# Kernel tuning notes

Measured on AMD Instinct MI355X. Metric: run time of the kernel, lower is better.

Reference implementation:

```python
import jax, jax.numpy as jnp
import numpy as np

N = 100000
E = 1600000
D_IN = 50
D_H = 128
D_OUT = 128
EPS = 1e-5


def setup_inputs() -> dict:
    key = jax.random.key(0)
    ks = jax.random.split(key, 24)
    def w(k, shape, fan_in):
        return jax.random.normal(k, shape, jnp.float32) / np.sqrt(fan_in)
    inp = {
        'x': jax.random.normal(ks[0], (N, D_IN), jnp.float32),
        'edge_src': jax.random.randint(ks[1], (E,), 0, N, jnp.int32),
        'edge_dst': jax.random.randint(ks[2], (E,), 0, N, jnp.int32),
        # SAGEConv 1: D_IN -> D_H
        'Wl1': w(ks[3], (D_IN, D_H), D_IN), 'Wr1': w(ks[4], (D_IN, D_H), D_IN), 'b1': jnp.zeros((D_H,), jnp.float32),
        # SAGEConv 2: D_H -> D_H
        'Wl2': w(ks[5], (D_H, D_H), D_H), 'Wr2': w(ks[6], (D_H, D_H), D_H), 'b2': jnp.zeros((D_H,), jnp.float32),
        # SAGEConv 3: D_H -> D_OUT
        'Wl3': w(ks[7], (D_H, D_OUT), D_H), 'Wr3': w(ks[8], (D_H, D_OUT), D_H), 'b3': jnp.zeros((D_OUT,), jnp.float32),
        # skip linears (no bias)
        'Ws1': w(ks[9], (D_IN, D_H), D_IN), 'Ws2': w(ks[10], (D_IN, D_H), D_IN),
        # LayerNorm affine
        'lnw1': jnp.ones((D_H,), jnp.float32), 'lnb1': jnp.zeros((D_H,), jnp.float32),
        'lnw2': jnp.ones((D_H,), jnp.float32), 'lnb2': jnp.zeros((D_H,), jnp.float32),
        'lnw3': jnp.ones((D_OUT,), jnp.float32), 'lnb3': jnp.zeros((D_OUT,), jnp.float32),
        # PReLU scalar slopes (PyG init 0.25)
        'a1': jnp.float32(0.25), 'a2': jnp.float32(0.25), 'a3': jnp.float32(0.25),
    }
    return inp


def _sage(x, src, dst, Wl, Wr, b):
    # mean aggregation of source features at destinations, then linear + root
    msg = x[src]                                              # [E, d]
    agg = jax.ops.segment_sum(msg, dst, num_segments=N)       # [N, d]
    cnt = jax.ops.segment_sum(jnp.ones((src.shape[0],), x.dtype), dst, num_segments=N)
    mean = agg / jnp.maximum(cnt, 1.0)[:, None]
    return mean @ Wl + x @ Wr + b


def _graph_ln(x, w, b):
    # PyG LayerNorm mode='graph', batch=None: normalize over all nodes+channels
    xc = x - jnp.mean(x)
    std = jnp.sqrt(jnp.mean(xc * xc))
    return (xc / (std + EPS)) * w + b


def _prelu(x, a):
    return jnp.where(x >= 0, x, a * x)


def reference(x, edge_src, edge_dst, Wl1, Wr1, b1, Wl2, Wr2, b2, Wl3, Wr3, b3,
              Ws1, Ws2, lnw1, lnb1, lnw2, lnb2, lnw3, lnb3, a1, a2, a3):
    h1 = _sage(x, edge_src, edge_dst, Wl1, Wr1, b1)
    h1 = _prelu(_graph_ln(h1, lnw1, lnb1), a1)
    h2 = _sage(h1 + x @ Ws1, edge_src, edge_dst, Wl2, Wr2, b2)
    h2 = _prelu(_graph_ln(h2, lnw2, lnb2), a2)
    ret = _sage(h1 + h2 + x @ Ws2, edge_src, edge_dst, Wl3, Wr3, b3)
    ret = _prelu(_graph_ln(ret, lnw3, lnb3), a3)
    return ret
```

## Files before the change

kernel.cpp:

```cpp
#include <hip/hip_runtime.h>

#define D_IN 50
#define LN_EPS 1e-5f
#define BSH 8
#define MAXB 512

typedef __bf16 bf16_t;
typedef bf16_t bf16x8 __attribute__((ext_vector_type(8)));
typedef bf16_t bf16x4 __attribute__((ext_vector_type(4)));
typedef bf16_t bf16x2 __attribute__((ext_vector_type(2)));
typedef float f32x4_t __attribute__((ext_vector_type(4)));

__global__ void bucket_hist_k(const int* __restrict__ dst, int* __restrict__ bcnt,
                              int e, int nb) {
    __shared__ int lh[MAXB];
    int t = threadIdx.x;
    for (int i = t; i < nb; i += 256) lh[i] = 0;
    __syncthreads();
    for (int i = blockIdx.x * 256 + t; i < e; i += gridDim.x * 256)
        atomicAdd(&lh[dst[i] >> BSH], 1);
    __syncthreads();
    for (int i = t; i < nb; i += 256) {
        int c = lh[i];
        if (c) atomicAdd(&bcnt[i * 16], c);
    }
}

__global__ void bscan_k(const int* __restrict__ bcnt, int* __restrict__ boff,
                        int* __restrict__ bpos, int nb, int e) {
    __shared__ int l[MAXB];
    int t = threadIdx.x;
    l[t] = (t < nb) ? bcnt[t * 16] : 0;
    __syncthreads();
    for (int off = 1; off < MAXB; off <<= 1) {
        int v = (t >= off) ? l[t - off] : 0;
        __syncthreads();
        l[t] += v;
        __syncthreads();
    }
    int excl = (t > 0) ? l[t - 1] : 0;
    if (t < nb) { boff[t] = excl; bpos[t * 16] = excl; }
    if (t == 0) boff[nb] = e;
}

__global__ void scatter_k(const int* __restrict__ src, const int* __restrict__ dst,
                          int* __restrict__ bpos, unsigned* __restrict__ pool,
                          int e, int nb) {
    __shared__ int lh[MAXB];
    __shared__ int lcur[MAXB];
    int t = threadIdx.x;
    for (int i = t; i < nb; i += 256) lh[i] = 0;
    __syncthreads();
    int chunk = (e + gridDim.x - 1) / gridDim.x;
    int s = blockIdx.x * chunk;
    int en = min(e, s + chunk);
    for (int i = s + t; i < en; i += 256)
        atomicAdd(&lh[dst[i] >> BSH], 1);
    __syncthreads();
    for (int i = t; i < nb; i += 256) {
        int c = lh[i];
        lcur[i] = c ? atomicAdd(&bpos[i * 16], c) : 0;
    }
    __syncthreads();
    for (int i = s + t; i < en; i += 256) {
        int d = dst[i];
        int p = atomicAdd(&lcur[d >> BSH], 1);
        pool[p] = (unsigned)src[i] | ((unsigned)(d & 255) << 17);
    }
}

__global__ void nhist_k(const unsigned* __restrict__ pool, const int* __restrict__ boff,
                        int* __restrict__ cnt, int n) {
    __shared__ int lc[256];
    int b = blockIdx.x, t = threadIdx.x;
    lc[t] = 0;
    __syncthreads();
    int s = boff[b], e = boff[b + 1];
    for (int i = s + t; i < e; i += 256) atomicAdd(&lc[pool[i] >> 17], 1);
    __syncthreads();
    int nd = (b << BSH) + t;
    if (nd < n) cnt[nd] = lc[t];
}

__global__ void scan_partial_k(const int* __restrict__ cnt, int* __restrict__ part, int n) {
    __shared__ int lds[256];
    int base = blockIdx.x * 1024;
    int t = threadIdx.x;
    int s = 0;
    for (int j = 0; j < 4; j++) {
        int idx = base + t * 4 + j;
        if (idx < n) s += cnt[idx];
    }
    lds[t] = s;
    __syncthreads();
    for (int off = 128; off > 0; off >>= 1) {
        if (t < off) lds[t] += lds[t + off];
        __syncthreads();
    }
    if (t == 0) part[blockIdx.x] = lds[0];
}

__global__ void scan_root_k(int* part, int nb) {
    if (threadIdx.x == 0 && blockIdx.x == 0) {
        int run = 0;
        for (int i = 0; i < nb; i++) { int v = part[i]; part[i] = run; run += v; }
    }
}

__global__ void scan_final_k(const int* __restrict__ cnt, const int* __restrict__ part,
                             int* __restrict__ row_ptr, int n) {
    __shared__ int lds[256];
    int base = blockIdx.x * 1024;
    int t = threadIdx.x;
    int v[4];
    int s = 0;
    for (int j = 0; j < 4; j++) {
        int idx = base + t * 4 + j;
        v[j] = (idx < n) ? cnt[idx] : 0;
        s += v[j];
    }
    lds[t] = s;
    __syncthreads();
    for (int off = 1; off < 256; off <<= 1) {
        int xv = (t >= off) ? lds[t - off] : 0;
        __syncthreads();
        lds[t] += xv;
        __syncthreads();
    }
    int ex = (t > 0 ? lds[t - 1] : 0) + part[blockIdx.x];
    for (int j = 0; j < 4; j++) {
        int idx = base + t * 4 + j;
        if (idx < n) {
            row_ptr[idx] = ex;
            if (idx == n - 1) row_ptr[n] = ex + v[j];
            ex += v[j];
        }
    }
}

__global__ void cfill_k(const unsigned* __restrict__ pool, const int* __restrict__ boff,
                        const int* __restrict__ rp, int* __restrict__ col, int n) {
    __shared__ int lpos[256];
    int b = blockIdx.x, t = threadIdx.x;
    int nd = (b << BSH) + t;
    lpos[t] = (nd < n) ? rp[nd] : 0;
    __syncthreads();
    int s = boff[b], e = boff[b + 1];
    for (int i = s + t; i < e; i += 256) {
        unsigned pk = pool[i];
        int slot = atomicAdd(&lpos[pk >> 17], 1);
        col[slot] = (int)(pk & 0x1FFFFu);
    }
}

struct ConvDesc { const float* w; bf16_t* o; int kin; int kpad; };
struct ConvArgs { ConvDesc d[8]; };

__global__ void conv_w_k(ConvArgs args) {
    ConvDesc d = args.d[blockIdx.y];
    int i = blockIdx.x * 256 + threadIdx.x;
    int tot = 128 * d.kpad;
    if (i >= tot) return;
    int n = i / d.kpad, k = i - n * d.kpad;
    float v = (k < d.kin) ? d.w[(size_t)k * 128 + n] : 0.f;
    d.o[i] = (bf16_t)v;
}

__global__ void conv_x_k(const float* __restrict__ x, bf16_t* __restrict__ xb, int n) {
    int i = blockIdx.x * 256 + threadIdx.x;
    if (i >= n * 64) return;
    int node = i >> 6, k = i & 63;
    xb[i] = (k < D_IN) ? (bf16_t)x[node * D_IN + k] : (bf16_t)0.f;
}

__global__ void agg_bf64_k(const bf16_t* __restrict__ feat, const int* __restrict__ rp,
                           const int* __restrict__ col, bf16_t* __restrict__ mean, int n) {
    int wid = (blockIdx.x * blockDim.x + threadIdx.x) >> 6;
    int lane = threadIdx.x & 63;
    if (wid >= n) return;
    int start = rp[wid], end = rp[wid + 1];
    float a0 = 0.f, a1 = 0.f;
    int e = start;
    for (; e + 3 < end; e += 4) {
        int s0 = col[e], s1 = col[e + 1], s2 = col[e + 2], s3 = col[e + 3];
        float v0 = (float)feat[(size_t)s0 * 64 + lane];
        float v1 = (float)feat[(size_t)s1 * 64 + lane];
        float v2 = (float)feat[(size_t)s2 * 64 + lane];
        float v3 = (float)feat[(size_t)s3 * 64 + lane];
        a0 += v0 + v1;
        a1 += v2 + v3;
    }
    for (; e < end; e++) a0 += (float)feat[(size_t)col[e] * 64 + lane];
    int c = end - start;
    float invc = 1.f / (float)(c > 0 ? c : 1);
    mean[(size_t)wid * 64 + lane] = (bf16_t)((a0 + a1) * invc);
}

__global__ void agg_bf128_k(const bf16_t* __restrict__ feat, const int* __restrict__ rp,
                            const int* __restrict__ col, bf16_t* __restrict__ mean, int n) {
    int wid = (blockIdx.x * blockDim.x + threadIdx.x) >> 6;
    int lane = threadIdx.x & 63;
    if (wid >= n) return;
    int start = rp[wid], end = rp[wid + 1];
    float ax0 = 0.f, ay0 = 0.f, ax1 = 0.f, ay1 = 0.f;
    int e = start;
    for (; e + 3 < end; e += 4) {
        int s0 = col[e], s1 = col[e + 1], s2 = col[e + 2], s3 = col[e + 3];
        bf16x2 v0 = *(const bf16x2*)(feat + (size_t)s0 * 128 + lane * 2);
        bf16x2 v1 = *(const bf16x2*)(feat + (size_t)s1 * 128 + lane * 2);
        bf16x2 v2 = *(const bf16x2*)(feat + (size_t)s2 * 128 + lane * 2);
        bf16x2 v3 = *(const bf16x2*)(feat + (size_t)s3 * 128 + lane * 2);
        ax0 += (float)v0.x + (float)v1.x;
        ay0 += (float)v0.y + (float)v1.y;
        ax1 += (float)v2.x + (float)v3.x;
        ay1 += (float)v2.y + (float)v3.y;
    }
    for (; e < end; e++) {
        bf16x2 v0 = *(const bf16x2*)(feat + (size_t)col[e] * 128 + lane * 2);
        ax0 += (float)v0.x;
        ay0 += (float)v0.y;
    }
    int c = end - start;
    float invc = 1.f / (float)(c > 0 ? c : 1);
    bf16x2 o;
    o.x = (bf16_t)((ax0 + ax1) * invc);
    o.y = (bf16_t)((ay0 + ay1) * invc);
    *(bf16x2*)(mean + (size_t)wid * 128 + lane * 2) = o;
}

template <int KPAD, bool DUAL, bool ACC>
__global__ __launch_bounds__(256) void mfma_gemm_k(
    const bf16_t* __restrict__ A, const bf16_t* __restrict__ B,
    const bf16_t* __restrict__ WlT, const bf16_t* __restrict__ WrT,
    const float* __restrict__ bias,
    bf16_t* __restrict__ out, float2* __restrict__ partials, int M) {
    constexpr int KC = KPAD / 32;
    constexpr int WELE = 8 * KC * 64 * 8;
    __shared__ bf16_t lwl[WELE];
    __shared__ bf16_t lwr[DUAL ? WELE : 8];

    const int tid = threadIdx.x;
    for (int ch = tid; ch < 8 * KC * 64; ch += 256) {
        int nt = ch / (KC * 64);
        int rem = ch - nt * (KC * 64);
        int c = rem >> 6;
        int ln = rem & 63;
        int m = ln & 15, q = ln >> 4;
        size_t srcoff = (size_t)(nt * 16 + m) * KPAD + c * 32 + q * 8;
        *(bf16x8*)&lwl[ch * 8] = *(const bf16x8*)(WlT + srcoff);
        if (DUAL) *(bf16x8*)&lwr[ch * 8] = *(const bf16x8*)(WrT + srcoff);
    }
    __syncthreads();

    const int wid = blockIdx.x * 4 + (tid >> 6);
    const int lane = tid & 63;
    const int row0 = wid * 32;
    if (row0 >= M) return;
    const int m = lane & 15;
    const int q = lane >> 4;

    bf16x8 af[2][KC], bfr[DUAL ? 2 : 1][DUAL ? KC : 1];
#pragma unroll
    for (int s = 0; s < 2; s++) {
        const bf16_t* ar = A + (size_t)(row0 + s * 16 + m) * KPAD + q * 8;
#pragma unroll
        for (int c = 0; c < KC; c++) af[s][c] = *(const bf16x8*)(ar + c * 32);
        if (DUAL) {
            const bf16_t* br = B + (size_t)(row0 + s * 16 + m) * KPAD + q * 8;
#pragma unroll
            for (int c = 0; c < KC; c++) bfr[s][c] = *(const bf16x8*)(br + c * 32);
        }
    }

    float lsum = 0.f, lsum2 = 0.f;
#pragma unroll
    for (int nt = 0; nt < 8; nt++) {
        f32x4_t acc0 = {0.f, 0.f, 0.f, 0.f};
        f32x4_t acc1 = {0.f, 0.f, 0.f, 0.f};
#pragma unroll
        for (int c = 0; c < KC; c++) {
            bf16x8 w = *(const bf16x8*)&lwl[((nt * KC + c) * 64 + lane) * 8];
            acc0 = __builtin_amdgcn_mfma_f32_16x16x32_bf16(af[0][c], w, acc0, 0, 0, 0);
            acc1 = __builtin_amdgcn_mfma_f32_16x16x32_bf16(af[1][c], w, acc1, 0, 0, 0);
        }
        if (DUAL) {
#pragma unroll
            for (int c = 0; c < KC; c++) {
                bf16x8 w = *(const bf16x8*)&lwr[((nt * KC + c) * 64 + lane) * 8];
                acc0 = __builtin_amdgcn_mfma_f32_16x16x32_bf16(bfr[0][c], w, acc0, 0, 0, 0);
                acc1 = __builtin_amdgcn_mfma_f32_16x16x32_bf16(bfr[1][c], w, acc1, 0, 0, 0);
            }
        }
        float bv = bias ? bias[nt * 16 + m] : 0.f;
#pragma unroll
        for (int s = 0; s < 2; s++) {
            f32x4_t* ap = (s == 0) ? &acc0 : &acc1;
#pragma unroll
            for (int r = 0; r < 4; r++) {
                int row = row0 + s * 16 + q * 4 + r;
                if (row < M) {
                    float o = (*ap)[r] + bv;
                    out[(size_t)row * 128 + nt * 16 + m] = (bf16_t)o;
                    if (ACC) { lsum += o; lsum2 += o * o; }
                }
            }
        }
    }
    if (ACC) {
        for (int off = 32; off > 0; off >>= 1) {
            lsum += __shfl_down(lsum, off);
            lsum2 += __shfl_down(lsum2, off);
        }
        if (lane == 0) partials[wid] = make_float2(lsum, lsum2);
    }
}

__global__ void reduce_partials_k(const float2* __restrict__ p, int n,
                                  double* __restrict__ outp) {
    __shared__ double s1[256], s2[256];
    int t = threadIdx.x;
    double a = 0.0, b = 0.0;
    for (int i = t; i < n; i += 256) { a += (double)p[i].x; b += (double)p[i].y; }
    s1[t] = a; s2[t] = b;
    __syncthreads();
    for (int off = 128; off > 0; off >>= 1) {
        if (t < off) { s1[t] += s1[t + off]; s2[t] += s2[t + off]; }
        __syncthreads();
    }
    if (t == 0) { outp[0] = s1[0]; outp[1] = s2[0]; }
}

template <int MODE>
__global__ void ln_prelu_k(const bf16_t* __restrict__ pre, const bf16_t* __restrict__ h1in,
                           const bf16_t* __restrict__ s,
                           const float* __restrict__ lnw, const float* __restrict__ lnb,
                           const float* __restrict__ a_ptr, const double* __restrict__ acc,
                           void* __restrict__ out0v, void* __restrict__ out1v, int total) {
    int i = blockIdx.x * blockDim.x + threadIdx.x;
    if (i * 4 >= total) return;
    double cinv = 1.0 / (double)total;
    double mm = acc[0] * cinv;
    double var = acc[1] * cinv - mm * mm;
    float stdv = (float)sqrt(var > 0.0 ? var : 0.0);
    float scale = 1.0f / (stdv + LN_EPS);
    float mf = (float)mm;
    float a = a_ptr[0];
    int c4 = i & 31;
    float4 w = ((const float4*)lnw)[c4];
    float4 b = ((const float4*)lnb)[c4];
    bf16x4 p4 = ((const bf16x4*)pre)[i];
    float4 h;
    h.x = ((float)p4.x - mf) * scale * w.x + b.x;
    h.y = ((float)p4.y - mf) * scale * w.y + b.y;
    h.z = ((float)p4.z - mf) * scale * w.z + b.z;
    h.w = ((float)p4.w - mf) * scale * w.w + b.w;
    h.x = h.x >= 0.f ? h.x : a * h.x;
    h.y = h.y >= 0.f ? h.y : a * h.y;
    h.z = h.z >= 0.f ? h.z : a * h.z;
    h.w = h.w >= 0.f ? h.w : a * h.w;
    if (MODE == 1) {
        bf16x4 hb;
        hb.x = (bf16_t)h.x; hb.y = (bf16_t)h.y; hb.z = (bf16_t)h.z; hb.w = (bf16_t)h.w;
        ((bf16x4*)out0v)[i] = hb;
        bf16x4 sv = ((const bf16x4*)s)[i];
        bf16x4 tb;
        tb.x = (bf16_t)(h.x + (float)sv.x); tb.y = (bf16_t)(h.y + (float)sv.y);
        tb.z = (bf16_t)(h.z + (float)sv.z); tb.w = (bf16_t)(h.w + (float)sv.w);
        ((bf16x4*)out1v)[i] = tb;
    } else if (MODE == 2) {
        bf16x4 hv = ((const bf16x4*)h1in)[i];
        bf16x4 sv = ((const bf16x4*)s)[i];
        bf16x4 tb;
        tb.x = (bf16_t)((float)hv.x + h.x + (float)sv.x);
        tb.y = (bf16_t)((float)hv.y + h.y + (float)sv.y);
        tb.z = (bf16_t)((float)hv.z + h.z + (float)sv.z);
        tb.w = (bf16_t)((float)hv.w + h.w + (float)sv.w);
        ((bf16x4*)out0v)[i] = tb;
    } else {
        ((float4*)out0v)[i] = h;
    }
}

extern "C" void kernel_launch(void* const* d_in, const int* in_sizes, int n_in,
                              void* d_out, int out_size, void* d_ws, size_t ws_size,
                              hipStream_t stream) {
    const float* x    = (const float*)d_in[0];
    const int*   esrc = (const int*)d_in[1];
    const int*   edst = (const int*)d_in[2];
    const float* Wl1  = (const float*)d_in[3];
    const float* Wr1  = (const float*)d_in[4];
    const float* b1   = (const float*)d_in[5];
    const float* Wl2  = (const float*)d_in[6];
    const float* Wr2  = (const float*)d_in[7];
    const float* b2   = (const float*)d_in[8];
    const float* Wl3  = (const float*)d_in[9];
    const float* Wr3  = (const float*)d_in[10];
    const float* b3   = (const float*)d_in[11];
    const float* Ws1  = (const float*)d_in[12];
    const float* Ws2  = (const float*)d_in[13];
    const float* lnw1 = (const float*)d_in[14];
    const float* lnb1 = (const float*)d_in[15];
    const float* lnw2 = (const float*)d_in[16];
    const float* lnb2 = (const float*)d_in[17];
    const float* lnw3 = (const float*)d_in[18];
    const float* lnb3 = (const float*)d_in[19];
    const float* a1   = (const float*)d_in[20];
    const float* a2   = (const float*)d_in[21];
    const float* a3   = (const float*)d_in[22];

    const int N = in_sizes[0] / D_IN;
    const int E = in_sizes[1];
    const int NB = (N + 255) >> BSH;

    char* ws = (char*)d_ws;
    size_t off = 0;
    auto alloc = [&](size_t bytes) -> void* {
        void* p = ws + off;
        off += (bytes + 255) & ~(size_t)255;
        return p;
    };
    bf16_t* xb   = (bf16_t*)alloc((size_t)N * 64 * 2);
    bf16_t* mean = (bf16_t*)alloc((size_t)N * 128 * 2);
    bf16_t* PRE  = (bf16_t*)alloc((size_t)N * 128 * 2);
    bf16_t* C    = (bf16_t*)alloc((size_t)N * 128 * 2);
    bf16_t* h1b  = (bf16_t*)alloc((size_t)N * 128 * 2);
    bf16_t* TB   = (bf16_t*)alloc((size_t)N * 128 * 2);
    bf16_t* WT   = (bf16_t*)alloc((size_t)(4 * 128 * 64 + 4 * 128 * 128) * 2);
    int* cnt  = (int*)alloc((size_t)N * 4);
    int* rp   = (int*)alloc((size_t)(N + 1) * 4);
    int* col  = (int*)alloc((size_t)E * 4);
    int* part = (int*)alloc(512);
    int* bcnt = (int*)alloc((size_t)MAXB * 16 * 4);
    int* boff = (int*)alloc((size_t)(MAXB + 1) * 4);
    int* bpos = (int*)alloc((size_t)MAXB * 16 * 4);
    unsigned* pool = (unsigned*)alloc((size_t)E * 4);
    double* lnacc = (double*)alloc(6 * 8);
    const int tiles = (N + 31) / 32;
    float2* partials = (float2*)alloc((size_t)tiles * 8);

    bf16_t* Wl1T = WT;
    bf16_t* Wr1T = Wl1T + 128 * 64;
    bf16_t* Ws1T = Wr1T + 128 * 64;
    bf16_t* Ws2T = Ws1T + 128 * 64;
    bf16_t* Wl2T = Ws2T + 128 * 64;
    bf16_t* Wr2T = Wl2T + 128 * 128;
    bf16_t* Wl3T = Wr2T + 128 * 128;
    bf16_t* Wr3T = Wl3T + 128 * 128;

    hipMemsetAsync(bcnt, 0, (size_t)MAXB * 16 * 4, stream);

    const int NBS_n = (N + 1023) / 1024;
    bucket_hist_k<<<256, 256, 0, stream>>>(edst, bcnt, E, NB);
    bscan_k<<<1, MAXB, 0, stream>>>(bcnt, boff, bpos, NB, E);
    scatter_k<<<256, 256, 0, stream>>>(esrc, edst, bpos, pool, E, NB);
    nhist_k<<<NB, 256, 0, stream>>>(pool, boff, cnt, N);
    scan_partial_k<<<NBS_n, 256, 0, stream>>>(cnt, part, N);
    scan_root_k<<<1, 64, 0, stream>>>(part, NBS_n);
    scan_final_k<<<NBS_n, 256, 0, stream>>>(cnt, part, rp, N);
    cfill_k<<<NB, 256, 0, stream>>>(pool, boff, rp, col, N);

    ConvArgs ca;
    ca.d[0] = {Wl1, Wl1T, 50, 64};
    ca.d[1] = {Wr1, Wr1T, 50, 64};
    ca.d[2] = {Ws1, Ws1T, 50, 64};
    ca.d[3] = {Ws2, Ws2T, 50, 64};
    ca.d[4] = {Wl2, Wl2T, 128, 128};
    ca.d[5] = {Wr2, Wr2T, 128, 128};
    ca.d[6] = {Wl3, Wl3T, 128, 128};
    ca.d[7] = {Wr3, Wr3T, 128, 128};
    conv_w_k<<<dim3(64, 8), 256, 0, stream>>>(ca);
    conv_x_k<<<(N * 64 + 255) / 256, 256, 0, stream>>>(x, xb, N);

    const int aggBlocks = ((N * 64) + 255) / 256;
    const int gemmBlocks = (tiles + 3) / 4;
    const int lnBlocks = (N * 128 / 4 + 255) / 256;
    const int total = N * 128;

    agg_bf64_k<<<aggBlocks, 256, 0, stream>>>(xb, rp, col, mean, N);
    mfma_gemm_k<64, true, true><<<gemmBlocks, 256, 0, stream>>>(
        mean, xb, Wl1T, Wr1T, b1, PRE, partials, N);
    reduce_partials_k<<<1, 256, 0, stream>>>(partials, tiles, lnacc + 0);
    mfma_gemm_k<64, false, false><<<gemmBlocks, 256, 0, stream>>>(
        xb, nullptr, Ws1T, nullptr, nullptr, C, nullptr, N);
    ln_prelu_k<1><<<lnBlocks, 256, 0, stream>>>(
        PRE, nullptr, C, lnw1, lnb1, a1, lnacc + 0, h1b, TB, total);

    agg_bf128_k<<<aggBlocks, 256, 0, stream>>>(TB, rp, col, mean, N);
    mfma_gemm_k<64, false, false><<<gemmBlocks, 256, 0, stream>>>(
        xb, nullptr, Ws2T, nullptr, nullptr, C, nullptr, N);
    mfma_gemm_k<128, true, true><<<gemmBlocks, 256, 0, stream>>>(
        mean, TB, Wl2T, Wr2T, b2, PRE, partials, N);
    reduce_partials_k<<<1, 256, 0, stream>>>(partials, tiles, lnacc + 2);
    ln_prelu_k<2><<<lnBlocks, 256, 0, stream>>>(
        PRE, h1b, C, lnw2, lnb2, a2, lnacc + 2, TB, nullptr, total);

    agg_bf128_k<<<aggBlocks, 256, 0, stream>>>(TB, rp, col, mean, N);
    mfma_gemm_k<128, true, true><<<gemmBlocks, 256, 0, stream>>>(
        mean, TB, Wl3T, Wr3T, b3, PRE, partials, N);
    reduce_partials_k<<<1, 256, 0, stream>>>(partials, tiles, lnacc + 4);
    ln_prelu_k<3><<<lnBlocks, 256, 0, stream>>>(
        PRE, nullptr, nullptr, lnw3, lnb3, a3, lnacc + 4, d_out, nullptr, total);
}
```

Before: 613.5 us.

## Vectorize mean-aggregation gathers and fuse layer-1 and skip GEMMs into one kernel

The aggregation kernels now split each wavefront into edge groups. Each lane loads 8 bf16 values (16 bytes) per neighbor instead of 1 or 2, and the groups' partial sums are combined with xor shuffles. This cuts the number of gather instructions and widens memory transactions. Separately, a new GEMM kernel computes the layer-1 SAGE output together with both skip projections (x@Ws1, x@Ws2) from a single load of xb, removing two GEMM launches and repeated reads of x. The cost is an extra buffer and more shared memory and registers per block.

```diff
diff --git a/kernel.cpp b/kernel.cpp
--- a/kernel.cpp
+++ b/kernel.cpp
@@ -179,21 +179,30 @@
     int lane = threadIdx.x & 63;
     if (wid >= n) return;
     int start = rp[wid], end = rp[wid + 1];
-    float a0 = 0.f, a1 = 0.f;
-    int e = start;
-    for (; e + 3 < end; e += 4) {
-        int s0 = col[e], s1 = col[e + 1], s2 = col[e + 2], s3 = col[e + 3];
-        float v0 = (float)feat[(size_t)s0 * 64 + lane];
-        float v1 = (float)feat[(size_t)s1 * 64 + lane];
-        float v2 = (float)feat[(size_t)s2 * 64 + lane];
-        float v3 = (float)feat[(size_t)s3 * 64 + lane];
-        a0 += v0 + v1;
-        a1 += v2 + v3;
-    }
-    for (; e < end; e++) a0 += (float)feat[(size_t)col[e] * 64 + lane];
+    int lc = lane & 7;
+    int g = lane >> 3;
+    float acc[8];
+#pragma unroll
+    for (int k = 0; k < 8; k++) acc[k] = 0.f;
+    for (int e = start + g; e < end; e += 8) {
+        int s0 = col[e];
+        bf16x8 v = *(const bf16x8*)(feat + (size_t)s0 * 64 + lc * 8);
+#pragma unroll
+        for (int k = 0; k < 8; k++) acc[k] += (float)v[k];
+    }
+#pragma unroll
+    for (int off = 8; off < 64; off <<= 1) {
+#pragma unroll
+        for (int k = 0; k < 8; k++) acc[k] += __shfl_xor(acc[k], off);
+    }
     int c = end - start;
     float invc = 1.f / (float)(c > 0 ? c : 1);
-    mean[(size_t)wid * 64 + lane] = (bf16_t)((a0 + a1) * invc);
+    if (lane < 8) {
+        bf16x8 o;
+#pragma unroll
+        for (int k = 0; k < 8; k++) o[k] = (bf16_t)(acc[k] * invc);
+        *(bf16x8*)(mean + (size_t)wid * 64 + lc * 8) = o;
+    }
 }
 
 __global__ void agg_bf128_k(const bf16_t* __restrict__ feat, const int* __restrict__ rp,
@@ -202,30 +211,30 @@
     int lane = threadIdx.x & 63;
     if (wid >= n) return;
     int start = rp[wid], end = rp[wid + 1];
-    float ax0 = 0.f, ay0 = 0.f, ax1 = 0.f, ay1 = 0.f;
-    int e = start;
-    for (; e + 3 < end; e += 4) {
-        int s0 = col[e], s1 = col[e + 1], s2 = col[e + 2], s3 = col[e + 3];
-        bf16x2 v0 = *(const bf16x2*)(feat + (size_t)s0 * 128 + lane * 2);
-        bf16x2 v1 = *(const bf16x2*)(feat + (size_t)s1 * 128 + lane * 2);
-        bf16x2 v2 = *(const bf16x2*)(feat + (size_t)s2 * 128 + lane * 2);
-        bf16x2 v3 = *(const bf16x2*)(feat + (size_t)s3 * 128 + lane * 2);
-        ax0 += (float)v0.x + (float)v1.x;
-        ay0 += (float)v0.y + (float)v1.y;
-        ax1 += (float)v2.x + (float)v3.x;
-        ay1 += (float)v2.y + (float)v3.y;
-    }
-    for (; e < end; e++) {
-        bf16x2 v0 = *(const bf16x2*)(feat + (size_t)col[e] * 128 + lane * 2);
-        ax0 += (float)v0.x;
-        ay0 += (float)v0.y;
+    int lc = lane & 15;
+    int g = lane >> 4;
+    float acc[8];
+#pragma unroll
+    for (int k = 0; k < 8; k++) acc[k] = 0.f;
+    for (int e = start + g; e < end; e += 4) {
+        int s0 = col[e];
+        bf16x8 v = *(const bf16x8*)(feat + (size_t)s0 * 128 + lc * 8);
+#pragma unroll
+        for (int k = 0; k < 8; k++) acc[k] += (float)v[k];
+    }
+#pragma unroll
+    for (int off = 16; off < 64; off <<= 1) {
+#pragma unroll
+        for (int k = 0; k < 8; k++) acc[k] += __shfl_xor(acc[k], off);
     }
     int c = end - start;
     float invc = 1.f / (float)(c > 0 ? c : 1);
-    bf16x2 o;
-    o.x = (bf16_t)((ax0 + ax1) * invc);
-    o.y = (bf16_t)((ay0 + ay1) * invc);
-    *(bf16x2*)(mean + (size_t)wid * 128 + lane * 2) = o;
+    if (lane < 16) {
+        bf16x8 o;
+#pragma unroll
+        for (int k = 0; k < 8; k++) o[k] = (bf16_t)(acc[k] * invc);
+        *(bf16x8*)(mean + (size_t)wid * 128 + lc * 8) = o;
+    }
 }
 
 template <int KPAD, bool DUAL, bool ACC>
@@ -313,6 +322,103 @@
         }
         if (lane == 0) partials[wid] = make_float2(lsum, lsum2);
     }
+}
+
+__global__ __launch_bounds__(256) void mfma_gemm3_k(
+    const bf16_t* __restrict__ A, const bf16_t* __restrict__ B,
+    const bf16_t* __restrict__ WlT, const bf16_t* __restrict__ WrT,
+    const bf16_t* __restrict__ Ws1T, const bf16_t* __restrict__ Ws2T,
+    const float* __restrict__ bias,
+    bf16_t* __restrict__ outP, bf16_t* __restrict__ outC1, bf16_t* __restrict__ outC2,
+    float2* __restrict__ partials, int M) {
+    constexpr int KC = 2;
+    constexpr int WELE = 8 * KC * 64 * 8;
+    __shared__ bf16_t lwl[WELE];
+    __shared__ bf16_t lwr[WELE];
+    __shared__ bf16_t ls1[WELE];
+    __shared__ bf16_t ls2[WELE];
+
+    const int tid = threadIdx.x;
+    for (int ch = tid; ch < 8 * KC * 64; ch += 256) {
+        int nt = ch / (KC * 64);
+        int rem = ch - nt * (KC * 64);
+        int c = rem >> 6;
+        int ln = rem & 63;
+        int m = ln & 15, q = ln >> 4;
+        size_t srcoff = (size_t)(nt * 16 + m) * 64 + c * 32 + q * 8;
+        *(bf16x8*)&lwl[ch * 8] = *(const bf16x8*)(WlT + srcoff);
+        *(bf16x8*)&lwr[ch * 8] = *(const bf16x8*)(WrT + srcoff);
+        *(bf16x8*)&ls1[ch * 8] = *(const bf16x8*)(Ws1T + srcoff);
+        *(bf16x8*)&ls2[ch * 8] = *(const bf16x8*)(Ws2T + srcoff);
+    }
+    __syncthreads();
+
+    const int wid = blockIdx.x * 4 + (tid >> 6);
+    const int lane = tid & 63;
+    const int row0 = wid * 32;
+    if (row0 >= M) return;
+    const int m = lane & 15;
+    const int q = lane >> 4;
+
+    bf16x8 af[2][KC], bfr[2][KC];
+#pragma unroll
+    for (int s = 0; s < 2; s++) {
+        const bf16_t* ar = A + (size_t)(row0 + s * 16 + m) * 64 + q * 8;
+        const bf16_t* br = B + (size_t)(row0 + s * 16 + m) * 64 + q * 8;
+#pragma unroll
+        for (int c = 0; c < KC; c++) {
+            af[s][c] = *(const bf16x8*)(ar + c * 32);
+            bfr[s][c] = *(const bf16x8*)(br + c * 32);
+        }
+    }
+
+    float lsum = 0.f, lsum2 = 0.f;
+#pragma unroll
+    for (int nt = 0; nt < 8; nt++) {
+        f32x4_t aP0 = {0.f, 0.f, 0.f, 0.f}, aP1 = {0.f, 0.f, 0.f, 0.f};
+        f32x4_t a10 = {0.f, 0.f, 0.f, 0.f}, a11 = {0.f, 0.f, 0.f, 0.f};
+        f32x4_t a20 = {0.f, 0.f, 0.f, 0.f}, a21 = {0.f, 0.f, 0.f, 0.f};
+#pragma unroll
+        for (int c = 0; c < KC; c++) {
+            int wi = ((nt * KC + c) * 64 + lane) * 8;
+            bf16x8 wl = *(const bf16x8*)&lwl[wi];
+            bf16x8 wr = *(const bf16x8*)&lwr[wi];
+            bf16x8 w1 = *(const bf16x8*)&ls1[wi];
+            bf16x8 w2 = *(const bf16x8*)&ls2[wi];
+            aP0 = __builtin_amdgcn_mfma_f32_16x16x32_bf16(af[0][c], wl, aP0, 0, 0, 0);
+            aP1 = __builtin_amdgcn_mfma_f32_16x16x32_bf16(af[1][c], wl, aP1, 0, 0, 0);
+            aP0 = __builtin_amdgcn_mfma_f32_16x16x32_bf16(bfr[0][c], wr, aP0, 0, 0, 0);
+            aP1 = __builtin_amdgcn_mfma_f32_16x16x32_bf16(bfr[1][c], wr, aP1, 0, 0, 0);
+            a10 = __builtin_amdgcn_mfma_f32_16x16x32_bf16(bfr[0][c], w1, a10, 0, 0, 0);
+            a11 = __builtin_amdgcn_mfma_f32_16x16x32_bf16(bfr[1][c], w1, a11, 0, 0, 0);
+            a20 = __builtin_amdgcn_mfma_f32_16x16x32_bf16(bfr[0][c], w2, a20, 0, 0, 0);
+            a21 = __builtin_amdgcn_mfma_f32_16x16x32_bf16(bfr[1][c], w2, a21, 0, 0, 0);
+        }
+        float bv = bias[nt * 16 + m];
+#pragma unroll
+        for (int s = 0; s < 2; s++) {
+            f32x4_t* pP = (s == 0) ? &aP0 : &aP1;
+            f32x4_t* p1 = (s == 0) ? &a10 : &a11;
+            f32x4_t* p2 = (s == 0) ? &a20 : &a21;
+#pragma unroll
+            for (int r = 0; r < 4; r++) {
+                int row = row0 + s * 16 + q * 4 + r;
+                if (row < M) {
+                    float o = (*pP)[r] + bv;
+                    size_t oi = (size_t)row * 128 + nt * 16 + m;
+                    outP[oi] = (bf16_t)o;
+                    outC1[oi] = (bf16_t)(*p1)[r];
+                    outC2[oi] = (bf16_t)(*p2)[r];
+                    lsum += o; lsum2 += o * o;
+                }
+            }
+        }
+    }
+    for (int off = 32; off > 0; off >>= 1) {
+        lsum += __shfl_down(lsum, off);
+        lsum2 += __shfl_down(lsum2, off);
+    }
+    if (lane == 0) partials[wid] = make_float2(lsum, lsum2);
 }
 
 __global__ void reduce_partials_k(const float2* __restrict__ p, int n,
@@ -422,7 +528,8 @@
     bf16_t* xb   = (bf16_t*)alloc((size_t)N * 64 * 2);
     bf16_t* mean = (bf16_t*)alloc((size_t)N * 128 * 2);
     bf16_t* PRE  = (bf16_t*)alloc((size_t)N * 128 * 2);
-    bf16_t* C    = (bf16_t*)alloc((size_t)N * 128 * 2);
+    bf16_t* C1   = (bf16_t*)alloc((size_t)N * 128 * 2);
+    bf16_t* C2   = (bf16_t*)alloc((size_t)N * 128 * 2);
     bf16_t* h1b  = (bf16_t*)alloc((size_t)N * 128 * 2);
     bf16_t* TB   = (bf16_t*)alloc((size_t)N * 128 * 2);
     bf16_t* WT   = (bf16_t*)alloc((size_t)(4 * 128 * 64 + 4 * 128 * 128) * 2);
@@ -477,22 +584,18 @@
     const int total = N * 128;
 
     agg_bf64_k<<<aggBlocks, 256, 0, stream>>>(xb, rp, col, mean, N);
-    mfma_gemm_k<64, true, true><<<gemmBlocks, 256, 0, stream>>>(
-        mean, xb, Wl1T, Wr1T, b1, PRE, partials, N);
+    mfma_gemm3_k<<<gemmBlocks, 256, 0, stream>>>(
+        mean, xb, Wl1T, Wr1T, Ws1T, Ws2T, b1, PRE, C1, C2, partials, N);
     reduce_partials_k<<<1, 256, 0, stream>>>(partials, tiles, lnacc + 0);
-    mfma_gemm_k<64, false, false><<<gemmBlocks, 256, 0, stream>>>(
-        xb, nullptr, Ws1T, nullptr, nullptr, C, nullptr, N);
     ln_prelu_k<1><<<lnBlocks, 256, 0, stream>>>(
-        PRE, nullptr, C, lnw1, lnb1, a1, lnacc + 0, h1b, TB, total);
+        PRE, nullptr, C1, lnw1, lnb1, a1, lnacc + 0, h1b, TB, total);
 
     agg_bf128_k<<<aggBlocks, 256, 0, stream>>>(TB, rp, col, mean, N);
-    mfma_gemm_k<64, false, false><<<gemmBlocks, 256, 0, stream>>>(
-        xb, nullptr, Ws2T, nullptr, nullptr, C, nullptr, N);
     mfma_gemm_k<128, true, true><<<gemmBlocks, 256, 0, stream>>>(
         mean, TB, Wl2T, Wr2T, b2, PRE, partials, N);
     reduce_partials_k<<<1, 256, 0, stream>>>(partials, tiles, lnacc + 2);
     ln_prelu_k<2><<<lnBlocks, 256, 0, stream>>>(
-        PRE, h1b, C, lnw2, lnb2, a2, lnacc + 2, TB, nullptr, total);
+        PRE, h1b, C2, lnw2, lnb2, a2, lnacc + 2, TB, nullptr, total);
 
     agg_bf128_k<<<aggBlocks, 256, 0, stream>>>(TB, rp, col, mean, N);
     mfma_gemm_k<128, true, true><<<gemmBlocks, 256, 0, stream>>>(
```

After: 579.7 us. 1.06x faster.
